# Kernel optimization log

Hardware: AMD Instinct MI355X
Metric: run time of the kernel (lower is better)

## Reference

```python
import jax, jax.numpy as jnp
import numpy as np
from jax import lax

TEMPERATURE = 0.5
MOMENTUM = 0.9
EPS = 1e-12  # F.normalize eps

B, D, K = 8192, 512, 16384


def _l2norm(x):
    # matches F.normalize(p=2): x / max(||x||, eps)
    n = jnp.sqrt(jnp.sum(x * x, axis=-1, keepdims=True))
    return x / jnp.maximum(n, EPS)


def setup_inputs() -> dict:
    key = jax.random.key(0)
    k1, k2, k3 = jax.random.split(key, 3)
    embeddings = jax.random.normal(k1, (B, D), dtype=jnp.float32)
    cluster_ids = jax.random.randint(k2, (B,), 0, K, dtype=jnp.int64)
    prototypes = jax.random.normal(k3, (K, D), dtype=jnp.float32)
    return {"embeddings": embeddings, "cluster_ids": cluster_ids, "prototypes": prototypes}


def reference(embeddings, cluster_ids, prototypes):
    emb_n = _l2norm(embeddings)            # [B, D]
    proto_n = _l2norm(prototypes)          # [K, D]
    sim = jnp.einsum('bd,kd->bk', emb_n, proto_n) / TEMPERATURE  # [B, K]

    pos = jnp.take_along_axis(sim, cluster_ids[:, None], axis=1)  # [B, 1]
    # mask out the positive column, then stable logsumexp over negatives
    is_pos = jnp.arange(sim.shape[1])[None, :] == cluster_ids[:, None]  # [B, K]
    neg = jnp.where(is_pos, -jnp.inf, sim)
    lse = jax.scipy.special.logsumexp(neg, axis=1, keepdims=True)       # [B, 1]
    loss = jnp.mean(-pos + lse)

    # serial momentum EMA update (order-dependent for duplicate cluster ids)
    def step(protos, xc):
        x, c = xc
        row = MOMENTUM * protos[c] + (1.0 - MOMENTUM) * x
        return protos.at[c].set(row), None

    new_protos, _ = lax.scan(step, prototypes, (embeddings, cluster_ids))
    return loss, new_protos
```

## Files before the change

### kernel.cpp

```cpp
#include <hip/hip_runtime.h>
#include <hip/hip_bf16.h>


#define B_N 8192
#define D_N 512
#define K_N 16384
#define INV_T 2.0f
#define MOM 0.9f

#define BM 128
#define BKF 128
#define BTR 256
#define KSPLIT 4
#define NTILE 16
#define NCH 64
#define BUFB 32768
#define CAP 64

typedef __attribute__((ext_vector_type(8))) int intx8;
typedef __attribute__((ext_vector_type(4))) float floatx4;

__device__ __forceinline__ void gl_lds16(const void* g, void* lds) {
    __builtin_amdgcn_global_load_lds(
        (const __attribute__((address_space(1))) void*)g,
        (__attribute__((address_space(3))) void*)lds, 16, 0, 0);
}

__device__ __forceinline__ intx8 frag2(const unsigned char* rp, int o0, int o1) {
    intx8 v;
    ((int4*)&v)[0] = *(const int4*)(rp + o0);
    ((int4*)&v)[1] = *(const int4*)(rp + o1);
    return v;
}

__global__ void norm_kernel(const float* __restrict__ emb, const float* __restrict__ pro,
                            unsigned char* __restrict__ embq, unsigned char* __restrict__ proq,
                            float* __restrict__ rowsum, float* __restrict__ out) {
    if (blockIdx.x < 32) rowsum[blockIdx.x * 256 + threadIdx.x] = 0.0f;
    if (blockIdx.x == 32 && threadIdx.x == 0) out[0] = 0.0f;
    int row = blockIdx.x * 4 + (threadIdx.x >> 6);
    int lane = threadIdx.x & 63;
    const float* x;
    unsigned char* o;
    if (row < B_N) {
        x = emb + (size_t)row * D_N;
        o = embq + (size_t)row * D_N;
    } else {
        x = pro + (size_t)(row - B_N) * D_N;
        o = proq + (size_t)(row - B_N) * D_N;
    }
    const float4* xp = (const float4*)(x + lane * 8);
    float4 v0 = xp[0];
    float4 v1 = xp[1];
    float ss = v0.x * v0.x + v0.y * v0.y + v0.z * v0.z + v0.w * v0.w +
               v1.x * v1.x + v1.y * v1.y + v1.z * v1.z + v1.w * v1.w;
    #pragma unroll
    for (int of = 32; of; of >>= 1) ss += __shfl_xor(ss, of);
    float sc = 16.0f / fmaxf(sqrtf(ss), 1e-12f);
    int w0 = 0, w1 = 0;
    w0 = __builtin_amdgcn_cvt_pk_fp8_f32(v0.x * sc, v0.y * sc, w0, false);
    w0 = __builtin_amdgcn_cvt_pk_fp8_f32(v0.z * sc, v0.w * sc, w0, true);
    w1 = __builtin_amdgcn_cvt_pk_fp8_f32(v1.x * sc, v1.y * sc, w1, false);
    w1 = __builtin_amdgcn_cvt_pk_fp8_f32(v1.z * sc, v1.w * sc, w1, true);
    int2 st = {w0, w1};
    *(int2*)(o + lane * 8) = st;
}

__global__ void pos_kernel(const float* __restrict__ emb, const float* __restrict__ pro,
                           const int* __restrict__ cid, float* __restrict__ rowpos) {
    int b = blockIdx.x * 4 + (threadIdx.x >> 6);
    int lane = threadIdx.x & 63;
    int c = cid[b];
    const float4* ep = (const float4*)(emb + (size_t)b * D_N + lane * 8);
    const float4* pp = (const float4*)(pro + (size_t)c * D_N + lane * 8);
    float4 e0 = ep[0], e1 = ep[1], p0 = pp[0], p1 = pp[1];
    float dp = e0.x * p0.x + e0.y * p0.y + e0.z * p0.z + e0.w * p0.w +
               e1.x * p1.x + e1.y * p1.y + e1.z * p1.z + e1.w * p1.w;
    float ee = e0.x * e0.x + e0.y * e0.y + e0.z * e0.z + e0.w * e0.w +
               e1.x * e1.x + e1.y * e1.y + e1.z * e1.z + e1.w * e1.w;
    float qq = p0.x * p0.x + p0.y * p0.y + p0.z * p0.z + p0.w * p0.w +
               p1.x * p1.x + p1.y * p1.y + p1.z * p1.z + p1.w * p1.w;
    #pragma unroll
    for (int o = 32; o; o >>= 1) {
        dp += __shfl_xor(dp, o);
        ee += __shfl_xor(ee, o);
        qq += __shfl_xor(qq, o);
    }
    if (lane == 0)
        rowpos[b] = INV_T * dp / (fmaxf(sqrtf(ee), 1e-12f) * fmaxf(sqrtf(qq), 1e-12f));
}

#define FSTEP(CH)                                                                     \
    do {                                                                              \
        const int cc = tt * 4 + (CH);                                                 \
        const int bW = bR >= BUFB ? bR - BUFB : bR + 2 * BUFB;                        \
        if (tt < NTILE - 1 || (CH) < 2) {                                             \
                              \
            const unsigned char* s = bS + (size_t)(((cc + 2) >> 2) * BTR) * D_N +     \
                                     ((((CH) + 2) & 3) << 7);                         \
            unsigned char* d = Bs + bW + ldsW;                                        \
            _Pragma("unroll")                                                         \
            for (int p = 0; p < 4; p++)                                               \
                gl_lds16(s + (size_t)p * 64 * D_N, d + p * 8192);                     \
        }                                                                             \
        const unsigned char* rb = Bs + bR + (wn * 64 + lcol) * BKF;                   \
        intx8 bf2[2];                                                                 \
        bf2[0] = frag2(rb + 0 * (16 * BKF), fsw0, fsw1);                              \
        bf2[1] = frag2(rb + 1 * (16 * BKF), fsw0, fsw1);                              \
        asm volatile("s_waitcnt lgkmcnt(0)" ::: "memory");                            \
        __builtin_amdgcn_sched_barrier(0);                                            \
        __builtin_amdgcn_s_setprio(1);                                                \
        _Pragma("unroll")                                                             \
        for (int i = 0; i < 4; i++)                                                   \
            _Pragma("unroll")                                                         \
            for (int j = 0; j < 2; j++)                                               \
                acc[i][j] = __builtin_amdgcn_mfma_scale_f32_16x16x128_f8f6f4(         \
                    afr[(CH)][i], bf2[j], acc[i][j], 0, 0, 0, 0x7F7F7F7F, 0,          \
                    0x7F7F7F7F);                                                      \
        __builtin_amdgcn_s_setprio(0);                                                \
        bf2[0] = frag2(rb + 2 * (16 * BKF), fsw0, fsw1);                              \
        bf2[1] = frag2(rb + 3 * (16 * BKF), fsw0, fsw1);                              \
        asm volatile("s_waitcnt lgkmcnt(0)" ::: "memory");                            \
        __builtin_amdgcn_sched_barrier(0);                                            \
        __builtin_amdgcn_s_setprio(1);                                                \
        _Pragma("unroll")                                                             \
        for (int i = 0; i < 4; i++)                                                   \
            _Pragma("unroll")                                                         \
            for (int j = 0; j < 2; j++)                                               \
                acc[i][2 + j] = __builtin_amdgcn_mfma_scale_f32_16x16x128_f8f6f4(     \
                    afr[(CH)][i], bf2[j], acc[i][2 + j], 0, 0, 0, 0x7F7F7F7F, 0,      \
                    0x7F7F7F7F);                                                      \
        __builtin_amdgcn_s_setprio(0);                                                \
        if ((CH) == 3) {     \
            _Pragma("unroll")                                                         \
            for (int i = 0; i < 4; i++)                                               \
                _Pragma("unroll")                                                     \
                for (int j = 0; j < 4; j++)                                           \
                    _Pragma("unroll")                                                 \
                    for (int r = 0; r < 4; r++) {                                     \
                        rs[i * 4 + r] += __expf(acc[i][j][r] * (INV_T / 256.0f));     \
                        acc[i][j][r] = 0.0f;                                          \
                    }                                                                 \
        }                                                                             \
        if (tt < NTILE - 1 || (CH) < 2)                                               \
            asm volatile("s_waitcnt vmcnt(4)" ::: "memory");                          \
        else                                                                          \
            asm volatile("s_waitcnt vmcnt(0)" ::: "memory");                          \
        __builtin_amdgcn_s_barrier();                                                 \
        bR = bR == 2 * BUFB ? 0 : bR + BUFB;                                          \
    } while (0)

__global__ __launch_bounds__(512, 2) void flash_kernel(const unsigned char* __restrict__ embq,
                                                       const unsigned char* __restrict__ proq,
                                                       float* __restrict__ rowsum_g) {
    __shared__ __align__(16) unsigned char Bs[3 * BUFB];
    const int t = threadIdx.x;
    const int w = t >> 6, lane = t & 63;
    const int quad = lane >> 4, lcol = lane & 15;
    const int wm = w >> 2, wn = w & 3;
    const int rowBase = blockIdx.x * BM;
    const int kb = blockIdx.y * (K_N / KSPLIT);

    const int fsw0 = (((quad << 1) | 0) ^ (lcol & 7)) << 4;
    const int fsw1 = (((quad << 1) | 1) ^ (lcol & 7)) << 4;
    const int ldsW = w * 1024;

    const unsigned char* bS = proq + (size_t)(kb + w * 8 + (lane >> 3)) * D_N +
                              (((lane & 7) ^ ((lane >> 3) & 7)) << 4);

    floatx4 acc[4][4];
    float rs[16];
    #pragma unroll
    for (int i = 0; i < 4; i++)
        #pragma unroll
        for (int j = 0; j < 4; j++) {
            floatx4 z = {0.0f, 0.0f, 0.0f, 0.0f};
            acc[i][j] = z;
        }
    #pragma unroll
    for (int i = 0; i < 16; i++) rs[i] = 0.0f;

    intx8 afr[4][4];
    {
        const unsigned char* aBase =
            embq + (size_t)(rowBase + wm * 64 + lcol) * D_N + quad * 32;
        #pragma unroll
        for (int ch = 0; ch < 4; ch++)
            #pragma unroll
            for (int i = 0; i < 4; i++) {
                const unsigned char* p = aBase + (size_t)i * (16 * D_N) + (ch << 7);
                ((int4*)&afr[ch][i])[0] = *(const int4*)(p);
                ((int4*)&afr[ch][i])[1] = *(const int4*)(p + 16);
            }
    }
    #pragma unroll
    for (int p = 0; p < 4; p++)
        gl_lds16(bS + (size_t)p * 64 * D_N, Bs + p * 8192 + ldsW);
    #pragma unroll
    for (int p = 0; p < 4; p++)
        gl_lds16(bS + (size_t)p * 64 * D_N + BKF, Bs + BUFB + p * 8192 + ldsW);
    asm volatile("s_waitcnt vmcnt(4)" ::: "memory");
    __builtin_amdgcn_s_barrier();

    int bR = 0;
    for (int tt = 0; tt < NTILE; tt++) {
        FSTEP(0);
        FSTEP(1);
        FSTEP(2);
        FSTEP(3);
    }

    #pragma unroll
    for (int i = 0; i < 16; i++) {
        #pragma unroll
        for (int o = 1; o < 16; o <<= 1) rs[i] += __shfl_xor(rs[i], o);
    }
    if (lcol == 0) {
        #pragma unroll
        for (int i = 0; i < 4; i++)
            #pragma unroll
            for (int r = 0; r < 4; r++)
                atomicAdd(&rowsum_g[rowBase + wm * 64 + i * 16 + quad * 4 + r],
                          rs[i * 4 + r]);
    }
}

__global__ void loss_kernel(const float* __restrict__ rowsum, const float* __restrict__ rowpos,
                            float* __restrict__ out, int* __restrict__ cnt) {
    __shared__ float red[256];
    int t = threadIdx.x;
    int b = blockIdx.x * 256 + t;
    cnt[b * 2] = 0;
    cnt[b * 2 + 1] = 0;
    float p = rowpos[b];
    red[t] = logf(rowsum[b] - __expf(p)) - p;
    __syncthreads();
    for (int o = 128; o; o >>= 1) {
        if (t < o) red[t] += red[t + o];
        __syncthreads();
    }
    if (t == 0) atomicAdd(out, red[0] * (1.0f / (float)B_N));
}

__global__ void ema_count(const int* __restrict__ cid, int* __restrict__ cnt,
                          int* __restrict__ bucket) {
    int b = blockIdx.x * 256 + threadIdx.x;
    int c = cid[b];
    int slot = atomicAdd(&cnt[c], 1);
    if (slot < CAP) bucket[c * CAP + slot] = b;
}

__global__ void ema_apply(const float* __restrict__ emb, const float* __restrict__ pro,
                          const int* __restrict__ cnt, const int* __restrict__ bucket,
                          float* __restrict__ outp) {
    int k = blockIdx.x * 4 + (threadIdx.x >> 6);
    int lane = threadIdx.x & 63;
    int n = cnt[k];
    n = n < CAP ? n : CAP;
    const float4* pp = (const float4*)(pro + (size_t)k * D_N + lane * 8);
    float4 a0 = pp[0], a1 = pp[1];
    int myb = (lane < n) ? bucket[k * CAP + lane] : 0x7fffffff;
    for (int i = 0; i < n; i++) {
        int m = myb;
        #pragma unroll
        for (int o = 1; o < 64; o <<= 1) {
            int v = __shfl_xor(m, o);
            m = v < m ? v : m;
        }
        const float4* ep = (const float4*)(emb + (size_t)m * D_N + lane * 8);
        float4 e0 = ep[0], e1 = ep[1];
        a0.x = MOM * a0.x + (1.0f - MOM) * e0.x;
        a0.y = MOM * a0.y + (1.0f - MOM) * e0.y;
        a0.z = MOM * a0.z + (1.0f - MOM) * e0.z;
        a0.w = MOM * a0.w + (1.0f - MOM) * e0.w;
        a1.x = MOM * a1.x + (1.0f - MOM) * e1.x;
        a1.y = MOM * a1.y + (1.0f - MOM) * e1.y;
        a1.z = MOM * a1.z + (1.0f - MOM) * e1.z;
        a1.w = MOM * a1.w + (1.0f - MOM) * e1.w;
        if (myb == m) myb = 0x7fffffff;
    }
    float4* op = (float4*)(outp + (size_t)k * D_N + lane * 8);
    op[0] = a0;
    op[1] = a1;
}

extern "C" void kernel_launch(void* const* d_in, const int* in_sizes, int n_in,
                              void* d_out, int out_size, void* d_ws, size_t ws_size,
                              hipStream_t stream) {
    const float* emb = (const float*)d_in[0];
    const int* cid = (const int*)d_in[1];
    const float* pro = (const float*)d_in[2];
    float* out = (float*)d_out;

    char* ws = (char*)d_ws;
    unsigned char* embq = (unsigned char*)ws;
    unsigned char* proq = (unsigned char*)(ws + 4194304);
    float* rowsum = (float*)(ws + 12582912);
    float* rowpos = (float*)(ws + 12615680);
    int* cnt = (int*)(ws + 4194304);
    int* bucket = (int*)(ws + 4194304 + 65536);

    norm_kernel<<<(B_N + K_N) / 4, 256, 0, stream>>>(emb, pro, embq, proq, rowsum, out);
    pos_kernel<<<B_N / 4, 256, 0, stream>>>(emb, pro, cid, rowpos);
    flash_kernel<<<dim3(B_N / BM, KSPLIT), 512, 0, stream>>>(embq, proq, rowsum);
    loss_kernel<<<B_N / 256, 256, 0, stream>>>(rowsum, rowpos, out, cnt);
    ema_count<<<B_N / 256, 256, 0, stream>>>(cid, cnt, bucket);
    ema_apply<<<K_N / 4, 256, 0, stream>>>(emb, pro, cnt, bucket, out + 1);
}
```

Before: 211.1 us.

## Drop explicit LDS waits in MFMA steps and remap workgroups for cache locality

Removes the manual lgkmcnt(0) waits and sched_barriers between B-fragment LDS reads and MFMA groups. This lets the compiler interleave the second fragment loads with the first MFMA batch. It also remaps the linear workgroup id so that neighbouring workgroups (likely co-scheduled, possibly on the same XCD) share row tiles and K-splits, aiming for better L2 reuse. The risk is that the compiler may schedule the waits worse than the hand-placed ones, and the remap assumes the grid shape.

New measurement: 211.9 us. No clear change (+0.3%).

```diff
diff --git a/kernel.cpp b/kernel.cpp
--- a/kernel.cpp
+++ b/kernel.cpp
@@ -13,7 +13,6 @@
 #define BTR 256
 #define KSPLIT 4
 #define NTILE 16
-#define NCH 64
 #define BUFB 32768
 #define CAP 64
 
@@ -31,6 +30,11 @@
     ((int4*)&v)[0] = *(const int4*)(rp + o0);
     ((int4*)&v)[1] = *(const int4*)(rp + o1);
     return v;
+}
+
+__device__ __forceinline__ floatx4 mxfma(intx8 a, intx8 b, floatx4 c) {
+    return __builtin_amdgcn_mfma_scale_f32_16x16x128_f8f6f4(a, b, c, 0, 0, 0,
+                                                            0x7F7F7F7F, 0, 0x7F7F7F7F);
 }
 
 __global__ void norm_kernel(const float* __restrict__ emb, const float* __restrict__ pro,
@@ -104,32 +108,23 @@
                 gl_lds16(s + (size_t)p * 64 * D_N, d + p * 8192);                     \
         }                                                                             \
         const unsigned char* rb = Bs + bR + (wn * 64 + lcol) * BKF;                   \
-        intx8 bf2[2];                                                                 \
-        bf2[0] = frag2(rb + 0 * (16 * BKF), fsw0, fsw1);                              \
-        bf2[1] = frag2(rb + 1 * (16 * BKF), fsw0, fsw1);                              \
-        asm volatile("s_waitcnt lgkmcnt(0)" ::: "memory");                            \
-        __builtin_amdgcn_sched_barrier(0);                                            \
+        intx8 bfA0 = frag2(rb + 0 * (16 * BKF), fsw0, fsw1);                          \
+        intx8 bfA1 = frag2(rb + 1 * (16 * BKF), fsw0, fsw1);                          \
         __builtin_amdgcn_s_setprio(1);                                                \
         _Pragma("unroll")                                                             \
-        for (int i = 0; i < 4; i++)                                                   \
-            _Pragma("unroll")                                                         \
-            for (int j = 0; j < 2; j++)                                               \
-                acc[i][j] = __builtin_amdgcn_mfma_scale_f32_16x16x128_f8f6f4(         \
-                    afr[(CH)][i], bf2[j], acc[i][j], 0, 0, 0, 0x7F7F7F7F, 0,          \
-                    0x7F7F7F7F);                                                      \
+        for (int i = 0; i < 4; i++) {                                                 \
+            acc[i][0] = mxfma(afr[(CH)][i], bfA0, acc[i][0]);                         \
+            acc[i][1] = mxfma(afr[(CH)][i], bfA1, acc[i][1]);                         \
+        }                                                                             \
         __builtin_amdgcn_s_setprio(0);                                                \
-        bf2[0] = frag2(rb + 2 * (16 * BKF), fsw0, fsw1);                              \
-        bf2[1] = frag2(rb + 3 * (16 * BKF), fsw0, fsw1);                              \
-        asm volatile("s_waitcnt lgkmcnt(0)" ::: "memory");                            \
-        __builtin_amdgcn_sched_barrier(0);                                            \
+        intx8 bfB0 = frag2(rb + 2 * (16 * BKF), fsw0, fsw1);                          \
+        intx8 bfB1 = frag2(rb + 3 * (16 * BKF), fsw0, fsw1);                          \
         __builtin_amdgcn_s_setprio(1);                                                \
         _Pragma("unroll")                                                             \
-        for (int i = 0; i < 4; i++)                                                   \
-            _Pragma("unroll")                                                         \
-            for (int j = 0; j < 2; j++)                                               \
-                acc[i][2 + j] = __builtin_amdgcn_mfma_scale_f32_16x16x128_f8f6f4(     \
-                    afr[(CH)][i], bf2[j], acc[i][2 + j], 0, 0, 0, 0x7F7F7F7F, 0,      \
-                    0x7F7F7F7F);                                                      \
+        for (int i = 0; i < 4; i++) {                                                 \
+            acc[i][2] = mxfma(afr[(CH)][i], bfB0, acc[i][2]);                         \
+            acc[i][3] = mxfma(afr[(CH)][i], bfB1, acc[i][3]);                         \
+        }                                                                             \
         __builtin_amdgcn_s_setprio(0);                                                \
         if ((CH) == 3) {     \
             _Pragma("unroll")                                                         \
@@ -158,8 +153,12 @@
     const int w = t >> 6, lane = t & 63;
     const int quad = lane >> 4, lcol = lane & 15;
     const int wm = w >> 2, wn = w & 3;
-    const int rowBase = blockIdx.x * BM;
-    const int kb = blockIdx.y * (K_N / KSPLIT);
+
+    const int wgl = blockIdx.x + (int)gridDim.x * blockIdx.y;
+    const int byp = (wgl & 7) >> 1;
+    const int bxp = ((wgl >> 3) << 1) + (wgl & 1);
+    const int rowBase = bxp * BM;
+    const int kb = byp * (K_N / KSPLIT);
 
     const int fsw0 = (((quad << 1) | 0) ^ (lcol & 7)) << 4;
     const int fsw1 = (((quad << 1) | 1) ^ (lcol & 7)) << 4;
```
